# Optimization experiments

Hardware: AMD Instinct MI355X
Metric: run time of the kernel (lower is better)

Reference implementation:

```python
import jax, jax.numpy as jnp
import numpy as np

M, N = 64, 8192
IN_DIM, HID, OUT = 6, 256, 128


def _mlp3(x, params):
    # three Linear+ReLU layers
    for W, b in params:
        x = jax.nn.relu(x @ W + b)
    return x


def setup_inputs() -> dict:
    key = jax.random.key(0)
    ks = jax.random.split(key, 16)
    def lin(k, fan_in, fan_out):
        bound = 1.0 / np.sqrt(fan_in)
        kw, kb = jax.random.split(k)
        W = jax.random.uniform(kw, (fan_in, fan_out), jnp.float32, -bound, bound)
        b = jax.random.uniform(kb, (fan_out,), jnp.float32, -bound, bound)
        return W, b
    feat = jax.random.normal(ks[0], (M, N, IN_DIM), jnp.float32)
    eW1, eb1 = lin(ks[1], IN_DIM, HID)
    eW2, eb2 = lin(ks[2], HID, HID)
    eW3, eb3 = lin(ks[3], HID, HID)
    sW1, sb1 = lin(ks[4], HID, OUT)
    sW2, sb2 = lin(ks[5], OUT, OUT)
    sW3, sb3 = lin(ks[6], OUT, OUT)
    cW, cb = lin(ks[7], IN_DIM + HID + OUT, 1)
    return {
        'feat': feat,
        'eW1': eW1, 'eb1': eb1, 'eW2': eW2, 'eb2': eb2, 'eW3': eW3, 'eb3': eb3,
        'sW1': sW1, 'sb1': sb1, 'sW2': sW2, 'sb2': sb2, 'sW3': sW3, 'sb3': sb3,
        'cW': cW, 'cb': cb,
    }


def reference(feat, eW1, eb1, eW2, eb2, eW3, eb3,
              sW1, sb1, sW2, sb2, sW3, sb3, cW, cb):
    # embed MLP over all points: [M, N, HID]
    hidden = _mlp3(feat, [(eW1, eb1), (eW2, eb2), (eW3, eb3)])
    # max-pool over points within each bbox: [M, HID]
    pooled = jnp.max(hidden, axis=1)
    # segment MLP on pooled feature: [M, OUT]
    seg = _mlp3(pooled, [(sW1, sb1), (sW2, sb2), (sW3, sb3)])
    # concat [feat, hidden, seg broadcast over points]: [M, N, 6+HID+OUT]
    seg_tiled = jnp.broadcast_to(seg[:, None, :], (feat.shape[0], feat.shape[1], seg.shape[-1]))
    concat = jnp.concatenate([feat, hidden, seg_tiled], axis=-1)
    # classifier -> score [M, N]
    score = (concat @ cW)[..., 0] + cb[0]
    # per-bbox min/max rescale to [-1, 1]
    smin = jnp.min(score, axis=1, keepdims=True)
    smax = jnp.max(score, axis=1, keepdims=True)
    score = (score - smin) / (smax - smin) * 2.0 - 1.0
    return score
```

## Files before the change

### kernel.cpp

```cpp
#include <hip/hip_runtime.h>


typedef __attribute__((ext_vector_type(8))) short short8;
typedef __attribute__((ext_vector_type(4))) float f32x4;

#define THREADS 512

__device__ __forceinline__ unsigned short f2bf(float f) {
  union { float f; unsigned int u; } x; x.f = f;
  unsigned int r = x.u + 0x7fffu + ((x.u >> 16) & 1u);
  return (unsigned short)(r >> 16);
}

__global__ void pn_pack(const float* __restrict__ W1,
                        const float* __restrict__ W2,
                        const float* __restrict__ W3,
                        unsigned short* __restrict__ wp) {
  int e = blockIdx.x * 256 + threadIdx.x;
  const float* src; int Kreal, base, r;
  if (e < 8192)       { src = W1; Kreal = 6;   base = 0;     r = e; }
  else if (e < 73728) { src = W2; Kreal = 256; base = 8192;  r = e - 8192; }
  else                { src = W3; Kreal = 256; base = 73728; r = e - 73728; }
  int j   = r & 7;
  int col = (r >> 3) & 15;
  int hi  = (r >> 7) & 3;
  int ct  = (r >> 9) & 15;
  int s   = r >> 13;
  int k = s * 32 + hi * 8 + j;
  int c = ct * 16 + col;
  float v = (k < Kreal) ? src[k * 256 + c] : 0.0f;
  wp[base + r] = f2bf(v);
}

template<int KSTEPS, int HSTRIDE, bool SWZ>
__device__ __forceinline__ void gemm_T(const unsigned short* __restrict__ wpL,
                                       const unsigned short* hbuf,
                                       int cgrp, int pgrp, int l15, int hi,
                                       f32x4 (&acc)[4][4]) {
#pragma unroll
  for (int ks = 0; ks < KSTEPS; ++ks) {
    short8 afr[4], bfr[4];
#pragma unroll
    for (int cf = 0; cf < 4; ++cf) {
      int ct = cgrp * 4 + cf;
      afr[cf] = *(const short8*)(wpL + (((((ks * 16 + ct) * 4) + hi) * 16 + l15) << 3));
    }
#pragma unroll
    for (int pf = 0; pf < 4; ++pf) {
      int p = pgrp * 64 + pf * 16 + l15;
      int byteoff = (p * HSTRIDE + ks * 32 + hi * 8) * 2;
      if (SWZ) byteoff ^= (p & 7) << 4;
      bfr[pf] = *(const short8*)((const char*)hbuf + byteoff);
    }
#pragma unroll
    for (int cf = 0; cf < 4; ++cf)
#pragma unroll
      for (int pf = 0; pf < 4; ++pf)
        acc[cf][pf] = __builtin_amdgcn_mfma_f32_16x16x32_bf16(
            afr[cf], bfr[pf], acc[cf][pf], 0, 0, 0);
  }
}

__device__ __forceinline__ void epi_h(f32x4 (&acc)[4][4], unsigned short* dst,
                                      const float* bv,
                                      int cgrp, int pgrp, int l15, int hi) {
#pragma unroll
  for (int cf = 0; cf < 4; ++cf) {
    int c0 = cgrp * 64 + cf * 16 + hi * 4;
    float b0 = bv[c0], b1 = bv[c0 + 1], b2 = bv[c0 + 2], b3 = bv[c0 + 3];
#pragma unroll
    for (int pf = 0; pf < 4; ++pf) {
      int p = pgrp * 64 + pf * 16 + l15;
      f32x4 a = acc[cf][pf];
      unsigned long long w =
            (unsigned long long)f2bf(fmaxf(a[0] + b0, 0.0f))
          | ((unsigned long long)f2bf(fmaxf(a[1] + b1, 0.0f)) << 16)
          | ((unsigned long long)f2bf(fmaxf(a[2] + b2, 0.0f)) << 32)
          | ((unsigned long long)f2bf(fmaxf(a[3] + b3, 0.0f)) << 48);
      int byteoff = ((p * 256 + c0) * 2) ^ ((p & 7) << 4);
      *(unsigned long long*)((char*)dst + byteoff) = w;
    }
  }
}

__global__ __launch_bounds__(THREADS, 1) void pn_main(
    const float* __restrict__ feat,
    const unsigned short* __restrict__ wp,
    const float* __restrict__ b1,
    const float* __restrict__ b2,
    const float* __restrict__ b3,
    const float* __restrict__ cW,
    float* __restrict__ out) {
  __shared__ unsigned short hA[128 * 256];
  __shared__ unsigned short hB[128 * 256];
  __shared__ unsigned short hF[128 * 40];
  __shared__ float fRaw[128 * 6];
  __shared__ float biasL[3 * 256];
  __shared__ float whL[256];
  __shared__ float sPart[4][128];

  const int tid  = threadIdx.x;
  const int lane = tid & 63;
  const int wave = tid >> 6;
  const int l15  = lane & 15;
  const int hi   = lane >> 4;
  const int cgrp = wave & 3;
  const int pgrp = wave >> 2;

  const int blk = blockIdx.x;
  const int m   = blk >> 6;
  const int n0  = (blk & 63) << 7;
  const int g0  = m * 8192 + n0;

  for (int i = tid; i < 768; i += THREADS) fRaw[i] = feat[g0 * 6 + i];
  if (tid < 256) {
    biasL[tid]       = b1[tid];
    biasL[256 + tid] = b2[tid];
    biasL[512 + tid] = b3[tid];
    whL[tid]         = cW[6 + tid];
  }
  __syncthreads();

  {
    int p = tid >> 2, ch = tid & 3;
    short8 vv;
#pragma unroll
    for (int jj = 0; jj < 8; ++jj) {
      int k = ch * 8 + jj;
      vv[jj] = (k < 6) ? (short)f2bf(fRaw[p * 6 + k]) : (short)0;
    }
    *(short8*)(hF + p * 40 + ch * 8) = vv;
  }
  __syncthreads();

  f32x4 acc[4][4];
  const f32x4 zz = {0.f, 0.f, 0.f, 0.f};

#pragma unroll
  for (int a = 0; a < 4; ++a)
#pragma unroll
    for (int b = 0; b < 4; ++b) acc[a][b] = zz;
  gemm_T<1, 40, false>(wp + 0, hF, cgrp, pgrp, l15, hi, acc);
  epi_h(acc, hA, biasL + 0, cgrp, pgrp, l15, hi);
  __syncthreads();

#pragma unroll
  for (int a = 0; a < 4; ++a)
#pragma unroll
    for (int b = 0; b < 4; ++b) acc[a][b] = zz;
  gemm_T<8, 256, true>(wp + 8192, hA, cgrp, pgrp, l15, hi, acc);
  epi_h(acc, hB, biasL + 256, cgrp, pgrp, l15, hi);
  __syncthreads();

#pragma unroll
  for (int a = 0; a < 4; ++a)
#pragma unroll
    for (int b = 0; b < 4; ++b) acc[a][b] = zz;
  gemm_T<8, 256, true>(wp + 73728, hB, cgrp, pgrp, l15, hi, acc);

  float part[4] = {0.f, 0.f, 0.f, 0.f};
#pragma unroll
  for (int cf = 0; cf < 4; ++cf) {
    int c0 = cgrp * 64 + cf * 16 + hi * 4;
#pragma unroll
    for (int r = 0; r < 4; ++r) {
      int c = c0 + r;
      float bb = biasL[512 + c];
      float wv = whL[c];
#pragma unroll
      for (int pf = 0; pf < 4; ++pf)
        part[pf] += fmaxf(acc[cf][pf][r] + bb, 0.0f) * wv;
    }
  }
#pragma unroll
  for (int off = 16; off < 64; off <<= 1)
#pragma unroll
    for (int pf = 0; pf < 4; ++pf)
      part[pf] += __shfl_xor(part[pf], off);
  if (hi == 0) {
#pragma unroll
    for (int pf = 0; pf < 4; ++pf)
      sPart[cgrp][pgrp * 64 + pf * 16 + l15] = part[pf];
  }
  __syncthreads();

  if (tid < 128) {
    int p = tid;
    float s = sPart[0][p] + sPart[1][p] + sPart[2][p] + sPart[3][p];
#pragma unroll
    for (int i = 0; i < 6; ++i) s += fRaw[p * 6 + i] * cW[i];
    out[g0 + p] = s;
  }
}

__global__ void pn_finalize(float* __restrict__ out) {
  __shared__ float smn[4], smx[4];
  int mrow = blockIdx.x;
  float* row = out + mrow * 8192;
  float v[32];
  float mn = 1e30f, mx = -1e30f;
#pragma unroll
  for (int i = 0; i < 32; ++i) {
    v[i] = row[threadIdx.x + i * 256];
    mn = fminf(mn, v[i]);
    mx = fmaxf(mx, v[i]);
  }
#pragma unroll
  for (int off = 1; off < 64; off <<= 1) {
    mn = fminf(mn, __shfl_xor(mn, off));
    mx = fmaxf(mx, __shfl_xor(mx, off));
  }
  int w = threadIdx.x >> 6;
  if ((threadIdx.x & 63) == 0) { smn[w] = mn; smx[w] = mx; }
  __syncthreads();
  mn = fminf(fminf(smn[0], smn[1]), fminf(smn[2], smn[3]));
  mx = fmaxf(fmaxf(smx[0], smx[1]), fmaxf(smx[2], smx[3]));
  float sc = 2.0f / (mx - mn);
#pragma unroll
  for (int i = 0; i < 32; ++i)
    row[threadIdx.x + i * 256] = (v[i] - mn) * sc - 1.0f;
}

extern "C" void kernel_launch(void* const* d_in, const int* in_sizes, int n_in,
                              void* d_out, int out_size, void* d_ws, size_t ws_size,
                              hipStream_t stream) {
  const float* feat = (const float*)d_in[0];
  const float* eW1  = (const float*)d_in[1];
  const float* eb1  = (const float*)d_in[2];
  const float* eW2  = (const float*)d_in[3];
  const float* eb2  = (const float*)d_in[4];
  const float* eW3  = (const float*)d_in[5];
  const float* eb3  = (const float*)d_in[6];
  const float* cW   = (const float*)d_in[13];
  float* out = (float*)d_out;
  unsigned short* wpack = (unsigned short*)d_ws;

  pn_pack<<<544, 256, 0, stream>>>(eW1, eW2, eW3, wpack);
  pn_main<<<4096, THREADS, 0, stream>>>(feat, wpack, eb1, eb2, eb3, cW, out);
  pn_finalize<<<64, 256, 0, stream>>>(out);
}
```

Baseline: 166.8 us.

## Shrink LDS footprint to one hidden buffer and raise occupancy

Drops the second 64KB hidden buffer and the raw-feature staging, reusing a single LDS activation buffer in place (with an extra barrier between the layer-2 GEMM and its epilogue), and raises launch_bounds occupancy from 1 to 4. The first layer now packs features into a compact 8-element row read only by the hi==0 lanes, and the per-point 6-wide classifier dot is computed in registers. Float-to-bf16 packing uses the hardware v_cvt_pk_bf16_f32 instruction. LDS per block falls from about 150KB to about 70KB, which lets two blocks share a CU, at the cost of an extra sync and tighter register limits that may cause spills.

```diff
diff --git a/kernel.cpp b/kernel.cpp
--- a/kernel.cpp
+++ b/kernel.cpp
@@ -3,6 +3,7 @@
 
 typedef __attribute__((ext_vector_type(8))) short short8;
 typedef __attribute__((ext_vector_type(4))) float f32x4;
+typedef __attribute__((ext_vector_type(4))) unsigned int u32x4;
 
 #define THREADS 512
 
@@ -10,6 +11,12 @@
   union { float f; unsigned int u; } x; x.f = f;
   unsigned int r = x.u + 0x7fffu + ((x.u >> 16) & 1u);
   return (unsigned short)(r >> 16);
+}
+
+__device__ __forceinline__ unsigned int cvt_pk_bf16(float lo, float hi) {
+  unsigned int r;
+  asm("v_cvt_pk_bf16_f32 %0, %1, %2" : "=v"(r) : "v"(lo), "v"(hi));
+  return r;
 }
 
 __global__ void pn_pack(const float* __restrict__ W1,
@@ -32,13 +39,12 @@
   wp[base + r] = f2bf(v);
 }
 
-template<int KSTEPS, int HSTRIDE, bool SWZ>
-__device__ __forceinline__ void gemm_T(const unsigned short* __restrict__ wpL,
-                                       const unsigned short* hbuf,
-                                       int cgrp, int pgrp, int l15, int hi,
-                                       f32x4 (&acc)[4][4]) {
-#pragma unroll
-  for (int ks = 0; ks < KSTEPS; ++ks) {
+__device__ __forceinline__ void gemm256(const unsigned short* __restrict__ wpL,
+                                        const unsigned short* hbuf,
+                                        int cgrp, int pgrp, int l15, int hi,
+                                        f32x4 (&acc)[4][4]) {
+#pragma unroll
+  for (int ks = 0; ks < 8; ++ks) {
     short8 afr[4], bfr[4];
 #pragma unroll
     for (int cf = 0; cf < 4; ++cf) {
@@ -48,8 +54,7 @@
 #pragma unroll
     for (int pf = 0; pf < 4; ++pf) {
       int p = pgrp * 64 + pf * 16 + l15;
-      int byteoff = (p * HSTRIDE + ks * 32 + hi * 8) * 2;
-      if (SWZ) byteoff ^= (p & 7) << 4;
+      int byteoff = ((p * 256 + ks * 32 + hi * 8) * 2) ^ ((p & 7) << 4);
       bfr[pf] = *(const short8*)((const char*)hbuf + byteoff);
     }
 #pragma unroll
@@ -72,18 +77,16 @@
     for (int pf = 0; pf < 4; ++pf) {
       int p = pgrp * 64 + pf * 16 + l15;
       f32x4 a = acc[cf][pf];
-      unsigned long long w =
-            (unsigned long long)f2bf(fmaxf(a[0] + b0, 0.0f))
-          | ((unsigned long long)f2bf(fmaxf(a[1] + b1, 0.0f)) << 16)
-          | ((unsigned long long)f2bf(fmaxf(a[2] + b2, 0.0f)) << 32)
-          | ((unsigned long long)f2bf(fmaxf(a[3] + b3, 0.0f)) << 48);
+      unsigned int lo  = cvt_pk_bf16(fmaxf(a[0] + b0, 0.0f), fmaxf(a[1] + b1, 0.0f));
+      unsigned int hi2 = cvt_pk_bf16(fmaxf(a[2] + b2, 0.0f), fmaxf(a[3] + b3, 0.0f));
+      unsigned long long w = (unsigned long long)lo | ((unsigned long long)hi2 << 32);
       int byteoff = ((p * 256 + c0) * 2) ^ ((p & 7) << 4);
       *(unsigned long long*)((char*)dst + byteoff) = w;
     }
   }
 }
 
-__global__ __launch_bounds__(THREADS, 1) void pn_main(
+__global__ __launch_bounds__(THREADS, 4) void pn_main(
     const float* __restrict__ feat,
     const unsigned short* __restrict__ wp,
     const float* __restrict__ b1,
@@ -92,12 +95,10 @@
     const float* __restrict__ cW,
     float* __restrict__ out) {
   __shared__ unsigned short hA[128 * 256];
-  __shared__ unsigned short hB[128 * 256];
-  __shared__ unsigned short hF[128 * 40];
-  __shared__ float fRaw[128 * 6];
+  __shared__ unsigned short hF[128 * 8];
   __shared__ float biasL[3 * 256];
   __shared__ float whL[256];
-  __shared__ float sPart[4][128];
+  float* sPart = (float*)hF;
 
   const int tid  = threadIdx.x;
   const int lane = tid & 63;
@@ -112,35 +113,54 @@
   const int n0  = (blk & 63) << 7;
   const int g0  = m * 8192 + n0;
 
-  for (int i = tid; i < 768; i += THREADS) fRaw[i] = feat[g0 * 6 + i];
   if (tid < 256) {
     biasL[tid]       = b1[tid];
     biasL[256 + tid] = b2[tid];
     biasL[512 + tid] = b3[tid];
     whL[tid]         = cW[6 + tid];
   }
-  __syncthreads();
-
-  {
-    int p = tid >> 2, ch = tid & 3;
-    short8 vv;
-#pragma unroll
-    for (int jj = 0; jj < 8; ++jj) {
-      int k = ch * 8 + jj;
-      vv[jj] = (k < 6) ? (short)f2bf(fRaw[p * 6 + k]) : (short)0;
-    }
-    *(short8*)(hF + p * 40 + ch * 8) = vv;
+
+  float fdot = 0.0f;
+  if (tid < 128) {
+    const float* fp = feat + (g0 + tid) * 6;
+    float f0 = fp[0], f1 = fp[1], f2 = fp[2], f3 = fp[3], f4 = fp[4], f5 = fp[5];
+    fdot = f0 * cW[0] + f1 * cW[1] + f2 * cW[2] + f3 * cW[3] + f4 * cW[4] + f5 * cW[5];
+    u32x4 v;
+    v[0] = cvt_pk_bf16(f0, f1);
+    v[1] = cvt_pk_bf16(f2, f3);
+    v[2] = cvt_pk_bf16(f4, f5);
+    v[3] = 0;
+    *(u32x4*)(hF + tid * 8) = v;
   }
   __syncthreads();
 
   f32x4 acc[4][4];
   const f32x4 zz = {0.f, 0.f, 0.f, 0.f};
+  const short8 zero8 = {0, 0, 0, 0, 0, 0, 0, 0};
 
 #pragma unroll
   for (int a = 0; a < 4; ++a)
 #pragma unroll
     for (int b = 0; b < 4; ++b) acc[a][b] = zz;
-  gemm_T<1, 40, false>(wp + 0, hF, cgrp, pgrp, l15, hi, acc);
+  {
+    short8 afr[4], bfr[4];
+#pragma unroll
+    for (int cf = 0; cf < 4; ++cf) {
+      int ct = cgrp * 4 + cf;
+      afr[cf] = *(const short8*)(wp + (((ct * 4 + hi) * 16 + l15) << 3));
+    }
+#pragma unroll
+    for (int pf = 0; pf < 4; ++pf) {
+      int p = pgrp * 64 + pf * 16 + l15;
+      bfr[pf] = (hi == 0) ? *(const short8*)(hF + p * 8) : zero8;
+    }
+#pragma unroll
+    for (int cf = 0; cf < 4; ++cf)
+#pragma unroll
+      for (int pf = 0; pf < 4; ++pf)
+        acc[cf][pf] = __builtin_amdgcn_mfma_f32_16x16x32_bf16(
+            afr[cf], bfr[pf], acc[cf][pf], 0, 0, 0);
+  }
   epi_h(acc, hA, biasL + 0, cgrp, pgrp, l15, hi);
   __syncthreads();
 
@@ -148,15 +168,16 @@
   for (int a = 0; a < 4; ++a)
 #pragma unroll
     for (int b = 0; b < 4; ++b) acc[a][b] = zz;
-  gemm_T<8, 256, true>(wp + 8192, hA, cgrp, pgrp, l15, hi, acc);
-  epi_h(acc, hB, biasL + 256, cgrp, pgrp, l15, hi);
+  gemm256(wp + 8192, hA, cgrp, pgrp, l15, hi, acc);
+  __syncthreads();
+  epi_h(acc, hA, biasL + 256, cgrp, pgrp, l15, hi);
   __syncthreads();
 
 #pragma unroll
   for (int a = 0; a < 4; ++a)
 #pragma unroll
     for (int b = 0; b < 4; ++b) acc[a][b] = zz;
-  gemm_T<8, 256, true>(wp + 73728, hB, cgrp, pgrp, l15, hi, acc);
+  gemm256(wp + 73728, hA, cgrp, pgrp, l15, hi, acc);
 
   float part[4] = {0.f, 0.f, 0.f, 0.f};
 #pragma unroll
@@ -180,16 +201,14 @@
   if (hi == 0) {
 #pragma unroll
     for (int pf = 0; pf < 4; ++pf)
-      sPart[cgrp][pgrp * 64 + pf * 16 + l15] = part[pf];
+      sPart[cgrp * 128 + pgrp * 64 + pf * 16 + l15] = part[pf];
   }
   __syncthreads();
 
   if (tid < 128) {
-    int p = tid;
-    float s = sPart[0][p] + sPart[1][p] + sPart[2][p] + sPart[3][p];
-#pragma unroll
-    for (int i = 0; i < 6; ++i) s += fRaw[p * 6 + i] * cW[i];
-    out[g0 + p] = s;
+    float s = sPart[tid] + sPart[128 + tid] + sPart[256 + tid] + sPart[384 + tid]
+            + fdot;
+    out[g0 + tid] = s;
   }
 }
 
```

After: 313.0 us. 87.7% more time.
